# Kernel tuning notes

Hardware: AMD Instinct MI355X
Metric: run time of the kernel (lower is better)

## Reference

```python
import jax, jax.numpy as jnp
import numpy as np
from functools import partial

N = 9
NN = N * N  # 81 cells
BTS = 4096
HID = 100


def build_constraint_mask():
    idx = np.arange(NN)
    r, c = idx // N, idx % N
    b = (r // 3) * 3 + (c // 3)
    row = (r[:, None] == r[None, :]).astype(np.float32)
    col = (c[:, None] == c[None, :]).astype(np.float32)
    box = (b[:, None] == b[None, :]).astype(np.float32)
    return jnp.asarray(np.stack([row, col, box], axis=1))  # [81, 3, 81]


def setup_inputs() -> dict:
    key = jax.random.key(0)
    k1, k2, k3, k4 = jax.random.split(key, 4)
    vals = jax.random.randint(k1, (BTS, NN), 0, N)
    filled = jax.random.uniform(k2, (BTS, NN)) < 0.4
    x = jax.nn.one_hot(vals, N, dtype=jnp.float32) * filled[:, :, None].astype(jnp.float32)
    W1 = jax.random.normal(k3, (HID, 3 * N), dtype=jnp.float32) * 0.1
    W2 = jax.random.normal(k4, (N, HID), dtype=jnp.float32) * 0.1
    return {"x": x, "W1": W1, "W2": W2, "constraint_mask": build_constraint_mask()}


def _sudoku_forward(x, W1, W2, cmask):
    bts = x.shape[0]
    b_idx = jnp.arange(bts)

    def step(carry, _):
        x, x_pred = carry
        # constraints[b,i,k,v] = sum_j cmask[i,k,j] * x[b,j,v]  -> [b,81,3,9]
        constraints = jnp.einsum('ikj,bjv->bikv', cmask, x)
        f = constraints.reshape(bts, NN, 3 * N)            # [b,81,27]
        h = jax.nn.relu(jnp.einsum('bif,hf->bih', f, W1))  # [b,81,100]
        y = jnp.einsum('bih,vh->biv', h, W2)               # [b,81,9]
        probs = jax.nn.softmax(y, axis=-1)
        empty = x.sum(-1) == 0                             # [b,81]
        x_pred = jnp.where(empty[..., None], probs, x_pred)
        s = jnp.where(empty[..., None], probs, 0.0)
        score = s.max(-1)                                  # [b,81]
        pos = jnp.argmax(s, -1)                            # [b,81]
        mmax = jnp.argmax(score, -1)                       # [b] best cell
        has_empty = empty.any(-1)                          # [b]
        sel_pos = pos[b_idx, mmax]
        newv = jnp.where(has_empty, 1.0, x[b_idx, mmax, sel_pos])
        x = x.at[b_idx, mmax, sel_pos].set(newv)
        return (x, x_pred), None

    # Original loops min_empty (max empties over batch) times; running the full
    # NN=81 steps is equivalent since iterations past a board's fill are no-ops.
    (x, x_pred), _ = jax.lax.scan(step, (x, x), None, length=NN)
    return x_pred, x


@jax.jit
def reference(x, W1, W2, constraint_mask):
    return _sudoku_forward(x, W1, W2, constraint_mask)
```

## Files before the change

### kernel.cpp

```cpp
#include <hip/hip_runtime.h>

#define TPB 256


__device__ __forceinline__ void fused_partial(
    int cell, int q, int slot,
    const double* __restrict__ H1, const float* __restrict__ W2T,
    double* __restrict__ pbuf)
{
    int r = cell / 9, c = cell - 9 * r;
    int bx = (r / 3) * 3 + c / 3;
    const double* Hr = H1 + r * 101;
    const double* Hc = H1 + (9 + c) * 101;
    const double* Hb = H1 + (18 + bx) * 101;
    double acc[9];
#pragma unroll
    for (int v = 0; v < 9; v++) acc[v] = 0.0;
    const int j0 = q * 20;
#pragma unroll 2
    for (int jj = 0; jj < 20; jj++) {
        int j = j0 + jj;
        double h = Hr[j] + Hc[j] + Hb[j];
        h = h > 0.0 ? h : 0.0;
        const float* w = W2T + j * 12;
#pragma unroll
        for (int v = 0; v < 9; v++) acc[v] = fma(h, (double)w[v], acc[v]);
    }
    double* pb = pbuf + (slot * 5 + q) * 9;
#pragma unroll
    for (int v = 0; v < 9; v++) pb[v] = acc[v];
}

__device__ __forceinline__ void combine_softmax(
    int cell, int slot,
    const double* __restrict__ pbuf,
    float* __restrict__ outp,
    double* __restrict__ score_l, int* __restrict__ pos_l)
{
    double y[9];
#pragma unroll
    for (int v = 0; v < 9; v++) {
        double s = 0.0;
#pragma unroll
        for (int q = 0; q < 5; q++) s += pbuf[(slot * 5 + q) * 9 + v];
        y[v] = s;
    }
    double m = y[0];
#pragma unroll
    for (int v = 1; v < 9; v++) m = fmax(m, y[v]);
    double p[9], sum = 0.0;
#pragma unroll
    for (int v = 0; v < 9; v++) { p[v] = exp(y[v] - m); sum += p[v]; }
    double inv = 1.0 / sum;
    double best = -1.0; int bv = 0;
#pragma unroll
    for (int v = 0; v < 9; v++) {
        double pr = p[v] * inv;
        outp[cell * 9 + v] = (float)pr;
        if (pr > best) { best = pr; bv = v; }
    }
    score_l[cell] = best;
    pos_l[cell] = bv;
}

__device__ __forceinline__ int affected_cell(int slot, int fr, int fc) {
    if (slot < 9)  return fr * 9 + slot;
    if (slot < 18) return (slot - 9) * 9 + fc;
    int r0 = (fr / 3) * 3, c0 = (fc / 3) * 3;
    int dr = fr - r0, dc = fc - c0;
    int rA = r0 + (dr == 0 ? 1 : 0), rB = r0 + (dr == 2 ? 1 : 2);
    int cA = c0 + (dc == 0 ? 1 : 0), cB = c0 + (dc == 2 ? 1 : 2);
    int k = slot - 18;
    return ((k < 2) ? rA : rB) * 9 + ((k & 1) ? cB : cA);
}

__global__ __launch_bounds__(TPB, 4) void sudoku_kernel(
    const float* __restrict__ x_in,
    const float* __restrict__ W1,
    const float* __restrict__ W2,
    float* __restrict__ out,
    int nb)
{
    const int b = blockIdx.x;
    const int t = threadIdx.x;

    __shared__ float  xs[729];
    __shared__ float  W2T[100 * 12];
    __shared__ float  cnt[27 * 12];
    __shared__ double H1[27 * 101];
    __shared__ double pbuf[22 * 5 * 9];
    __shared__ double score_l[81];
    __shared__ int    pos_l[81];
    __shared__ double red_s[2];
    __shared__ int    red_i[2];
    __shared__ int    bc_cell;

    float* outp = out + (size_t)b * 729;
    float* outx = out + (size_t)nb * 729 + (size_t)b * 729;
    const float* xb = x_in + (size_t)b * 729;

    for (int i = t; i < 729; i += TPB) { float v = xb[i]; xs[i] = v; outp[i] = v; }
    for (int i = t; i < 900; i += TPB) { int v = i / 100, j = i - 100 * v; W2T[j * 12 + v] = W2[i]; }
    __syncthreads();

    if (t < 81) {
        float s = 0.f;
#pragma unroll
        for (int v = 0; v < 9; v++) s += xs[t * 9 + v];
        score_l[t] = (s == 0.f) ? 0.0 : -1.0;
        pos_l[t] = 0;
    }
    for (int o = t; o < 243; o += TPB) {
        int g = o / 9, v = o - 9 * g;
        float s = 0.f;
        if (g < 9) {
            int base = g * 9;
#pragma unroll
            for (int k = 0; k < 9; k++) s += xs[(base + k) * 9 + v];
        } else if (g < 18) {
            int c = g - 9;
#pragma unroll
            for (int k = 0; k < 9; k++) s += xs[(c + 9 * k) * 9 + v];
        } else {
            int bx = g - 18;
            int base = (bx / 3) * 27 + (bx % 3) * 3;
#pragma unroll
            for (int k = 0; k < 9; k++) s += xs[(base + (k / 3) * 9 + (k % 3)) * 9 + v];
        }
        cnt[g * 12 + v] = s;
    }
    __syncthreads();

    for (int o = t; o < 2700; o += TPB) {
        int g = o / 100, j = o - 100 * g;
        int type = (g >= 18) ? 2 : (g >= 9 ? 1 : 0);
        const float* w = W1 + j * 27 + type * 9;
        const float* cc = cnt + g * 12;
        double s = 0.0;
#pragma unroll
        for (int v = 0; v < 9; v++) s = fma((double)w[v], (double)cc[v], s);
        H1[g * 101 + j] = s;
    }
    int myflag = (t < 81) ? (score_l[t] == 0.0) : 0;
    int ne = __syncthreads_count(myflag);

    for (int c0 = 0; c0 < 81; c0 += 22) {
        int slot = t % 22, q = t / 22;
        if (q < 5) {
            int cell = c0 + slot;
            if (cell < 81 && score_l[cell] == 0.0)
                fused_partial(cell, q, slot, H1, W2T, pbuf);
        }
        __syncthreads();
        if (t < 22) {
            int cell = c0 + t;
            if (cell < 81 && score_l[cell] == 0.0)
                combine_softmax(cell, t, pbuf, outp, score_l, pos_l);
        }
        __syncthreads();
    }

    for (; ne > 0; --ne) {
        if (t < 128) {
            double s; int i;
            if (t < 81) { s = score_l[t]; i = t; } else { s = -1.0; i = 127; }
#pragma unroll
            for (int off = 1; off < 64; off <<= 1) {
                double s2 = __shfl_xor(s, off);
                int    i2 = __shfl_xor(i, off);
                if (s2 > s || (s2 == s && i2 < i)) { s = s2; i = i2; }
            }
            if ((t & 63) == 0) { red_s[t >> 6] = s; red_i[t >> 6] = i; }
        }
        __syncthreads();
        if (t == 0) {
            double s1 = red_s[0]; int i1 = red_i[0];
            if (red_s[1] > s1) { s1 = red_s[1]; i1 = red_i[1]; }
            int cell = i1, bv = pos_l[cell];
            bc_cell = cell;
            xs[cell * 9 + bv] = 1.0f;
            score_l[cell] = -1.0;
            int r = cell / 9, c = cell - 9 * r;
            int bx = (r / 3) * 3 + c / 3;
            cnt[r * 12 + bv] += 1.f;
            cnt[(9 + c) * 12 + bv] += 1.f;
            cnt[(18 + bx) * 12 + bv] += 1.f;
        }
        __syncthreads();
        const int fcell = bc_cell;
        const int fr = fcell / 9, fc = fcell - 9 * fr;
        const int fbx = (fr / 3) * 3 + fc / 3;
        for (int o = t; o < 300; o += TPB) {
            int gi = o / 100, j = o - 100 * gi;
            int g = (gi == 0) ? fr : (gi == 1) ? (9 + fc) : (18 + fbx);
            const float* w = W1 + j * 27 + gi * 9;
            const float* cc = cnt + g * 12;
            double s = 0.0;
#pragma unroll
            for (int v = 0; v < 9; v++) s = fma((double)w[v], (double)cc[v], s);
            H1[g * 101 + j] = s;
        }
        __syncthreads();
        {
            int slot = t % 22, q = t / 22;
            if (q < 5) {
                int cell = affected_cell(slot, fr, fc);
                if (score_l[cell] >= 0.0)
                    fused_partial(cell, q, slot, H1, W2T, pbuf);
            }
        }
        __syncthreads();
        if (t < 22) {
            int cell = affected_cell(t, fr, fc);
            if (score_l[cell] >= 0.0)
                combine_softmax(cell, t, pbuf, outp, score_l, pos_l);
        }
        __syncthreads();
    }

    for (int i = t; i < 729; i += TPB) outx[i] = xs[i];
}

extern "C" void kernel_launch(void* const* d_in, const int* in_sizes, int n_in,
                              void* d_out, int out_size, void* d_ws, size_t ws_size,
                              hipStream_t stream) {
    const float* x  = (const float*)d_in[0];
    const float* W1 = (const float*)d_in[1];
    const float* W2 = (const float*)d_in[2];
    int nb = in_sizes[0] / 729;
    (void)n_in; (void)out_size; (void)d_ws; (void)ws_size;
    sudoku_kernel<<<nb, TPB, 0, stream>>>(x, W1, W2, (float*)d_out, nb);
}
```

Baseline: 1.319 ms.

## Widen per-cell work split, parallelize softmax, single-wave argmax, stage x_pred in LDS

Splits the hidden dimension for each cell across 9 thread groups of 12 instead of 5 of 20, so 198 threads do the layer-2 partial sums. The softmax combine is spread across 9 lanes per cell (one per value) using wave barriers, rather than a single thread per cell. The argmax over 81 cells now runs inside one wave and drops a block sync. x_pred is also kept in LDS and written to global once at the end instead of being scattered during the loop. Together these aim to shorten the serial critical path of each step, at the cost of more shared memory and lane-level sync.

```diff
diff --git a/kernel.cpp b/kernel.cpp
--- a/kernel.cpp
+++ b/kernel.cpp
@@ -3,8 +3,18 @@
 #define TPB 256
 
 
-__device__ __forceinline__ void fused_partial(
-    int cell, int q, int slot,
+__device__ __forceinline__ int affected_cell(int slot, int fr, int fc) {
+    if (slot < 9)  return fr * 9 + slot;
+    if (slot < 18) return (slot - 9) * 9 + fc;
+    int r0 = (fr / 3) * 3, c0 = (fc / 3) * 3;
+    int dr = fr - r0, dc = fc - c0;
+    int rA = r0 + (dr == 0 ? 1 : 0), rB = r0 + (dr == 2 ? 1 : 2);
+    int cA = c0 + (dc == 0 ? 1 : 0), cB = c0 + (dc == 2 ? 1 : 2);
+    int k = slot - 18;
+    return ((k < 2) ? rA : rB) * 9 + ((k & 1) ? cB : cA);
+}
+
+__device__ __forceinline__ void do_F(int slot, int q, int cell,
     const double* __restrict__ H1, const float* __restrict__ W2T,
     double* __restrict__ pbuf)
 {
@@ -16,62 +26,53 @@
     double acc[9];
 #pragma unroll
     for (int v = 0; v < 9; v++) acc[v] = 0.0;
-    const int j0 = q * 20;
-#pragma unroll 2
-    for (int jj = 0; jj < 20; jj++) {
+    const int j0 = q * 12;
+#pragma unroll
+    for (int jj = 0; jj < 12; jj++) {
         int j = j0 + jj;
-        double h = Hr[j] + Hc[j] + Hb[j];
-        h = h > 0.0 ? h : 0.0;
-        const float* w = W2T + j * 12;
-#pragma unroll
-        for (int v = 0; v < 9; v++) acc[v] = fma(h, (double)w[v], acc[v]);
-    }
-    double* pb = pbuf + (slot * 5 + q) * 9;
+        if (j < 100) {
+            double h = Hr[j] + Hc[j] + Hb[j];
+            h = h > 0.0 ? h : 0.0;
+            const float* w = W2T + j * 12;
+#pragma unroll
+            for (int v = 0; v < 9; v++) acc[v] = fma(h, (double)w[v], acc[v]);
+        }
+    }
+    double* pb = pbuf + (slot * 9 + q) * 9;
 #pragma unroll
     for (int v = 0; v < 9; v++) pb[v] = acc[v];
 }
 
-__device__ __forceinline__ void combine_softmax(
-    int cell, int slot,
-    const double* __restrict__ pbuf,
-    float* __restrict__ outp,
+__device__ __forceinline__ void do_C(int slot, int v, int cell,
+    const double* __restrict__ pbuf, double* __restrict__ ybuf,
+    double* __restrict__ pexp, float* __restrict__ xp,
     double* __restrict__ score_l, int* __restrict__ pos_l)
 {
-    double y[9];
-#pragma unroll
-    for (int v = 0; v < 9; v++) {
-        double s = 0.0;
-#pragma unroll
-        for (int q = 0; q < 5; q++) s += pbuf[(slot * 5 + q) * 9 + v];
-        y[v] = s;
-    }
-    double m = y[0];
-#pragma unroll
-    for (int v = 1; v < 9; v++) m = fmax(m, y[v]);
-    double p[9], sum = 0.0;
-#pragma unroll
-    for (int v = 0; v < 9; v++) { p[v] = exp(y[v] - m); sum += p[v]; }
-    double inv = 1.0 / sum;
-    double best = -1.0; int bv = 0;
-#pragma unroll
-    for (int v = 0; v < 9; v++) {
-        double pr = p[v] * inv;
-        outp[cell * 9 + v] = (float)pr;
-        if (pr > best) { best = pr; bv = v; }
-    }
-    score_l[cell] = best;
-    pos_l[cell] = bv;
-}
-
-__device__ __forceinline__ int affected_cell(int slot, int fr, int fc) {
-    if (slot < 9)  return fr * 9 + slot;
-    if (slot < 18) return (slot - 9) * 9 + fc;
-    int r0 = (fr / 3) * 3, c0 = (fc / 3) * 3;
-    int dr = fr - r0, dc = fc - c0;
-    int rA = r0 + (dr == 0 ? 1 : 0), rB = r0 + (dr == 2 ? 1 : 2);
-    int cA = c0 + (dc == 0 ? 1 : 0), cB = c0 + (dc == 2 ? 1 : 2);
-    int k = slot - 18;
-    return ((k < 2) ? rA : rB) * 9 + ((k & 1) ? cB : cA);
+    double y = 0.0;
+#pragma unroll
+    for (int q = 0; q < 9; q++) y += pbuf[(slot * 9 + q) * 9 + v];
+    ybuf[slot * 9 + v] = y;
+    __builtin_amdgcn_wave_barrier();
+    double m = ybuf[slot * 9 + 0];
+#pragma unroll
+    for (int v2 = 1; v2 < 9; v2++) m = fmax(m, ybuf[slot * 9 + v2]);
+    pexp[slot * 9 + v] = exp(y - m);
+    __builtin_amdgcn_wave_barrier();
+    if (v == 0) {
+        double sum = 0.0;
+#pragma unroll
+        for (int v2 = 0; v2 < 9; v2++) sum += pexp[slot * 9 + v2];
+        double inv = 1.0 / sum;
+        double best = -1.0; int bv = 0;
+#pragma unroll
+        for (int v2 = 0; v2 < 9; v2++) {
+            double pr = pexp[slot * 9 + v2] * inv;
+            xp[cell * 9 + v2] = (float)pr;
+            if (pr > best) { best = pr; bv = v2; }
+        }
+        score_l[cell] = best;
+        pos_l[cell] = bv;
+    }
 }
 
 __global__ __launch_bounds__(TPB, 4) void sudoku_kernel(
@@ -85,21 +86,19 @@
     const int t = threadIdx.x;
 
     __shared__ float  xs[729];
+    __shared__ float  xp[729];
     __shared__ float  W2T[100 * 12];
     __shared__ float  cnt[27 * 12];
     __shared__ double H1[27 * 101];
-    __shared__ double pbuf[22 * 5 * 9];
+    __shared__ double pbuf[22 * 9 * 9];
+    __shared__ double ybuf[22 * 9];
+    __shared__ double pexp[22 * 9];
     __shared__ double score_l[81];
     __shared__ int    pos_l[81];
-    __shared__ double red_s[2];
-    __shared__ int    red_i[2];
     __shared__ int    bc_cell;
 
-    float* outp = out + (size_t)b * 729;
-    float* outx = out + (size_t)nb * 729 + (size_t)b * 729;
     const float* xb = x_in + (size_t)b * 729;
-
-    for (int i = t; i < 729; i += TPB) { float v = xb[i]; xs[i] = v; outp[i] = v; }
+    for (int i = t; i < 729; i += TPB) { float v = xb[i]; xs[i] = v; xp[i] = v; }
     for (int i = t; i < 900; i += TPB) { int v = i / 100, j = i - 100 * v; W2T[j * 12 + v] = W2[i]; }
     __syncthreads();
 
@@ -145,51 +144,56 @@
     int ne = __syncthreads_count(myflag);
 
     for (int c0 = 0; c0 < 81; c0 += 22) {
-        int slot = t % 22, q = t / 22;
-        if (q < 5) {
+        if (t < 198) {
+            int slot = t % 22, q = t / 22;
             int cell = c0 + slot;
-            if (cell < 81 && score_l[cell] == 0.0)
-                fused_partial(cell, q, slot, H1, W2T, pbuf);
-        }
-        __syncthreads();
-        if (t < 22) {
-            int cell = c0 + t;
-            if (cell < 81 && score_l[cell] == 0.0)
-                combine_softmax(cell, t, pbuf, outp, score_l, pos_l);
-        }
-        __syncthreads();
-    }
-
-    for (; ne > 0; --ne) {
-        if (t < 128) {
-            double s; int i;
-            if (t < 81) { s = score_l[t]; i = t; } else { s = -1.0; i = 127; }
+            if (cell < 81 && score_l[cell] >= 0.0)
+                do_F(slot, q, cell, H1, W2T, pbuf);
+        }
+        __syncthreads();
+        {
+            int w = t >> 6, l = t & 63;
+            if (l < 63) {
+                int sw = l / 9, v = l - 9 * sw;
+                int slot = w * 7 + sw;
+                int cell = c0 + slot;
+                if (slot < 22 && cell < 81 && score_l[cell] >= 0.0)
+                    do_C(slot, v, cell, pbuf, ybuf, pexp, xp, score_l, pos_l);
+            }
+        }
+        __syncthreads();
+    }
+
+    for (int step = 0; step < ne; ++step) {
+        if (t < 64) {
+            double s = score_l[t]; int idx = t;
+            if (t < 17) {
+                double s2 = score_l[64 + t];
+                if (s2 > s) { s = s2; idx = 64 + t; }
+            }
 #pragma unroll
             for (int off = 1; off < 64; off <<= 1) {
                 double s2 = __shfl_xor(s, off);
-                int    i2 = __shfl_xor(i, off);
-                if (s2 > s || (s2 == s && i2 < i)) { s = s2; i = i2; }
-            }
-            if ((t & 63) == 0) { red_s[t >> 6] = s; red_i[t >> 6] = i; }
-        }
-        __syncthreads();
-        if (t == 0) {
-            double s1 = red_s[0]; int i1 = red_i[0];
-            if (red_s[1] > s1) { s1 = red_s[1]; i1 = red_i[1]; }
-            int cell = i1, bv = pos_l[cell];
-            bc_cell = cell;
-            xs[cell * 9 + bv] = 1.0f;
-            score_l[cell] = -1.0;
-            int r = cell / 9, c = cell - 9 * r;
-            int bx = (r / 3) * 3 + c / 3;
-            cnt[r * 12 + bv] += 1.f;
-            cnt[(9 + c) * 12 + bv] += 1.f;
-            cnt[(18 + bx) * 12 + bv] += 1.f;
+                int    i2 = __shfl_xor(idx, off);
+                if (s2 > s || (s2 == s && i2 < idx)) { s = s2; idx = i2; }
+            }
+            if (t == 0) {
+                int cell = idx, bv = pos_l[cell];
+                bc_cell = cell;
+                xs[cell * 9 + bv] = 1.0f;
+                score_l[cell] = -1.0;
+                int r = cell / 9, c = cell - 9 * r;
+                int bx = (r / 3) * 3 + c / 3;
+                cnt[r * 12 + bv] += 1.f;
+                cnt[(9 + c) * 12 + bv] += 1.f;
+                cnt[(18 + bx) * 12 + bv] += 1.f;
+            }
         }
         __syncthreads();
         const int fcell = bc_cell;
         const int fr = fcell / 9, fc = fcell - 9 * fr;
         const int fbx = (fr / 3) * 3 + fc / 3;
+
         for (int o = t; o < 300; o += TPB) {
             int gi = o / 100, j = o - 100 * gi;
             int g = (gi == 0) ? fr : (gi == 1) ? (9 + fc) : (18 + fbx);
@@ -201,24 +205,33 @@
             H1[g * 101 + j] = s;
         }
         __syncthreads();
+
+        if (t < 198) {
+            int slot = t % 22, q = t / 22;
+            int cell = affected_cell(slot, fr, fc);
+            if (score_l[cell] >= 0.0)
+                do_F(slot, q, cell, H1, W2T, pbuf);
+        }
+        __syncthreads();
+
         {
-            int slot = t % 22, q = t / 22;
-            if (q < 5) {
-                int cell = affected_cell(slot, fr, fc);
-                if (score_l[cell] >= 0.0)
-                    fused_partial(cell, q, slot, H1, W2T, pbuf);
-            }
-        }
-        __syncthreads();
-        if (t < 22) {
-            int cell = affected_cell(t, fr, fc);
-            if (score_l[cell] >= 0.0)
-                combine_softmax(cell, t, pbuf, outp, score_l, pos_l);
-        }
-        __syncthreads();
-    }
-
-    for (int i = t; i < 729; i += TPB) outx[i] = xs[i];
+            int w = t >> 6, l = t & 63;
+            if (l < 63) {
+                int sw = l / 9, v = l - 9 * sw;
+                int slot = w * 7 + sw;
+                if (slot < 22) {
+                    int cell = affected_cell(slot, fr, fc);
+                    if (score_l[cell] >= 0.0)
+                        do_C(slot, v, cell, pbuf, ybuf, pexp, xp, score_l, pos_l);
+                }
+            }
+        }
+        __syncthreads();
+    }
+
+    float* outp = out + (size_t)b * 729;
+    float* outx = out + (size_t)nb * 729 + (size_t)b * 729;
+    for (int i = t; i < 729; i += TPB) { outp[i] = xp[i]; outx[i] = xs[i]; }
 }
 
 extern "C" void kernel_launch(void* const* d_in, const int* in_sizes, int n_in,
```

After: 1.279 ms. -3.1%, faster.
